# Optimization experiments

Hardware: AMD Instinct MI355X
Metric: run time of the kernel (lower is better)

## Reference

```python
import jax, jax.numpy as jnp
import numpy as np
from jax import lax

VOCAB, E, T, B, LABELS = 50000, 256, 512, 32, 16


def setup_inputs() -> dict:
    key = jax.random.key(0)
    ks = jax.random.split(key, 10)
    inputs = jax.random.randint(ks[0], (B, T), 0, VOCAB)
    emb_table = jax.random.normal(ks[1], (VOCAB, E), jnp.float32) * 0.02
    # Original torch code samples fresh randn weights at every timestep:
    # faithful parameterization is a stacked [T, E, E] weight per matrix.
    Wl = jax.random.normal(ks[2], (T, E, E), jnp.float32)
    Wsl = jax.random.normal(ks[3], (T, E, E), jnp.float32)
    Wr = jax.random.normal(ks[4], (T, E, E), jnp.float32)
    Wsr = jax.random.normal(ks[5], (T, E, E), jnp.float32)
    e_prev0 = jax.random.normal(ks[6], (B, E), jnp.float32)   # embedding_previous init (randn)
    e_foll0 = jax.random.normal(ks[7], (B, E), jnp.float32)   # embedding_following init (randn)
    fc_w = jax.random.normal(ks[8], (LABELS, 3 * E), jnp.float32) * 0.02
    fc_b = jnp.zeros((LABELS,), jnp.float32)
    return {"inputs": inputs, "emb_table": emb_table, "Wl": Wl, "Wsl": Wsl,
            "Wr": Wr, "Wsr": Wsr, "e_prev0": e_prev0, "e_foll0": e_foll0,
            "fc_w": fc_w, "fc_b": fc_b}


def _context_scan(W, Ws, emb_seq, e0):
    # W, Ws: [T, E, E]; emb_seq: [T, B, E] (order in which embeddings feed the recurrence)
    # c_i = tanh(c_{i-1} @ W_i + e_prev @ Ws_i); e_prev starts at e0 then trails emb_seq.
    c0 = jnp.zeros_like(e0)

    def step(carry, xs):
        c_prev, e_prev = carry
        W_i, Ws_i, emb_i = xs
        c = jnp.tanh(c_prev @ W_i + e_prev @ Ws_i)
        return (c, emb_i), c

    _, ctx = lax.scan(step, (c0, e0), (W, Ws, emb_seq))
    return ctx  # [T, B, E]


def reference(inputs, emb_table, Wl, Wsl, Wr, Wsr, e_prev0, e_foll0, fc_w, fc_b):
    emb = emb_table[inputs]                 # [B, T, E]
    emb_t = jnp.transpose(emb, (1, 0, 2))   # [T, B, E]
    left = _context_scan(Wl, Wsl, emb_t, e_prev0)                 # [T, B, E]
    right = _context_scan(Wr, Wsr, emb_t[::-1], e_foll0)[::-1]    # [T, B, E] (reversed order)
    out = jnp.concatenate([left, emb_t, right], axis=-1)          # [T, B, 3E]
    out = jnp.transpose(out, (1, 0, 2))                           # [B, T, 3E]
    pooled = jnp.max(out, axis=1)                                 # [B, 3E]
    # dropout in eval mode: identity
    return pooled @ fc_w.T + fc_b                                 # [B, LABELS]
```

## Files before the change

kernel.cpp:

```cpp
#include <hip/hip_runtime.h>
#include <cstdint>
#include <cstddef>

#define T_ 512
#define B_ 32
#define E_ 256
#define NLAB 16

typedef __attribute__((ext_vector_type(8))) short short8;
typedef __attribute__((ext_vector_type(4))) float f32x4;
typedef __attribute__((ext_vector_type(16))) float f32x16;
typedef __attribute__((ext_vector_type(2))) long long2_t;
typedef __attribute__((ext_vector_type(4))) int int4v;
typedef __attribute__((ext_vector_type(8))) int int8v;

static __device__ __forceinline__ unsigned short f2bf(float f) {
    unsigned u = __float_as_uint(f);
    u = (u + 0x7fffu + ((u >> 16) & 1u)) >> 16;
    return (unsigned short)u;
}

static __device__ __forceinline__ unsigned f2fp8(float x) {
    unsigned u = __float_as_uint(x);
    unsigned sign = (u >> 31) << 7;
    unsigned mag = u & 0x7fffffffu;
    if (mag >= 0x43e00000u) return sign | 0x7eu;
    if (mag < 0x3c800000u) {
        float v = fabsf(x) * 512.0f;
        int r = (int)rintf(v);
        return sign | (unsigned)r;
    }
    unsigned lsb = (mag >> 20) & 1u;
    mag += 0x7ffffu + lsb;
    unsigned exp8 = mag >> 23;
    return sign | (((exp8 - 120u) << 3) | ((mag >> 20) & 7u));
}

static __device__ __forceinline__ unsigned pk_fp8(float a, float b) {
#if __has_builtin(__builtin_amdgcn_cvt_pk_fp8_f32)
    return (unsigned)__builtin_amdgcn_cvt_pk_fp8_f32(a, b, 0, false);
#else
    return f2fp8(a) | (f2fp8(b) << 8);
#endif
}
static __device__ __forceinline__ unsigned pk4_fp8(float a, float b, float c, float d) {
#if __has_builtin(__builtin_amdgcn_cvt_pk_fp8_f32)
    int lo = __builtin_amdgcn_cvt_pk_fp8_f32(a, b, 0, false);
    return (unsigned)__builtin_amdgcn_cvt_pk_fp8_f32(c, d, lo, true);
#else
    return f2fp8(a) | (f2fp8(b) << 8) | (f2fp8(c) << 16) | (f2fp8(d) << 24);
#endif
}

static __device__ __forceinline__ unsigned q4(float x) {
    float a = fabsf(x);
    unsigned c = (a >= 0.25f) + (a >= 0.75f) + (a >= 1.25f) + (a >= 1.75f) +
                 (a >= 2.5f) + (a >= 3.5f) + (a >= 5.0f);
    return c | ((__float_as_uint(x) >> 28) & 8u);
}

static __device__ __forceinline__ float sig_act(float x) {
    float d = __builtin_fmaf(x, x, 1.0f);
#if __has_builtin(__builtin_amdgcn_rsqf)
    float r = __builtin_amdgcn_rsqf(d);
#else
    float r = rsqrtf(d);
#endif
    return x * r;
}

static __device__ __forceinline__ short8 gather_bfrag_f32(const float* Wt, int kt, int nt, int lane) {
    const float* p = Wt + (size_t)(kt * 16 + 8 * (lane >> 5)) * E_ + nt * 32 + (lane & 31);
    short8 r;
#pragma unroll
    for (int j = 0; j < 8; ++j) {
        float v = __builtin_nontemporal_load(p);
        r[j] = (short)f2bf(v);
        p += E_;
    }
    return r;
}
static __device__ __forceinline__ short8 gather_afrag_rows(const float* rowbase, int kt, int lane) {
    const float* p = rowbase + kt * 16 + 8 * (lane >> 5);
    f32x4 v0 = *(const f32x4*)p;
    f32x4 v1 = *(const f32x4*)(p + 4);
    short8 r;
#pragma unroll
    for (int j = 0; j < 4; ++j) r[j] = (short)f2bf(v0[j]);
#pragma unroll
    for (int j = 0; j < 4; ++j) r[4 + j] = (short)f2bf(v1[j]);
    return r;
}
static __device__ __forceinline__ short8 lds_afrag_bf16(const unsigned short* c_buf, int kt, int lane) {
    int b = lane & 31;
    int byte = (b * 512 + (kt * 16 + 8 * (lane >> 5)) * 2) ^ ((b & 7) << 4);
    return *(const short8*)((const char*)c_buf + byte);
}

static __device__ __forceinline__ void produce_w(
        const float* __restrict__ Wl, const float* __restrict__ Wr,
        unsigned char* __restrict__ wfrag, int d, int t, int tid) {
    int lane = tid & 63, w = tid >> 6;
    const float* W = (d ? Wr : Wl) + (size_t)t * E_ * E_;
    int f = w * 32 + (lane & 31);
    int hh = lane >> 5;
    unsigned char* dst = wfrag + (size_t)(d * T_ + t) * 32768 + w * 4096 + lane * 16;
#pragma unroll
    for (int i = 0; i < 4; ++i) {
        const float* p = W + (size_t)(64 * i + 32 * hh) * E_ + f;
        int4v out;
#pragma unroll
        for (int dw = 0; dw < 4; ++dw) {
            unsigned v = 0;
#pragma unroll
            for (int b = 0; b < 4; ++b) {
                float v0 = __builtin_nontemporal_load(p + (size_t)(dw * 8 + 2 * b) * E_);
                float v1 = __builtin_nontemporal_load(p + (size_t)(dw * 8 + 2 * b + 1) * E_);
                v |= (q4(v0) | (q4(v1) << 4)) << (8 * b);
            }
            out[dw] = (int)v;
        }
        *(int4v*)(dst + i * 1024) = out;
    }
}
static __device__ __forceinline__ void produce_z(
        const int* __restrict__ inputs, const float* __restrict__ emb,
        const float* __restrict__ Wsl, const float* __restrict__ Wsr,
        const float* __restrict__ e_prev0, const float* __restrict__ e_foll0,
        unsigned char* __restrict__ zfrag, int d, int t, int tid) {
    int lane = tid & 63, w = tid >> 6;
    const float* Ws = (d ? Wsr : Wsl) + (size_t)t * E_ * E_;
    int b = lane & 31;
    const float* rowbase;
    if (t == 0) {
        rowbase = (d ? e_foll0 : e_prev0) + b * E_;
    } else {
        int tok = inputs[b * T_ + (d ? (T_ - t) : (t - 1))];
        rowbase = emb + (size_t)tok * E_;
    }
    f32x16 acc;
#pragma unroll
    for (int r = 0; r < 16; ++r) acc[r] = 0.0f;
#pragma unroll 2
    for (int kt = 0; kt < 16; ++kt) {
        short8 a = gather_afrag_rows(rowbase, kt, lane);
        short8 bf = gather_bfrag_f32(Ws, kt, w, lane);
        acc = __builtin_amdgcn_mfma_f32_32x32x16_bf16(a, bf, acc, 0, 0, 0);
    }
    unsigned char* zp = zfrag + (size_t)(d * T_ + t) * 8192 + w * 1024;
    int fb = lane & 31;
    int hc = (fb >> 3) & 1;
    int bytepos = (fb >> 4) * 8 + (fb & 7);
    int hz = lane >> 5;
#pragma unroll
    for (int q = 0; q < 8; ++q) {
        unsigned p2 = pk_fp8(acc[2 * q], acc[2 * q + 1]);
        int r0 = 2 * q, r1 = 2 * q + 1;
        int b0 = (r0 & 3) + 8 * (r0 >> 2) + 4 * hz;
        int b1 = (r1 & 3) + 8 * (r1 >> 2) + 4 * hz;
        zp[(32 * hc + b0) * 16 + bytepos] = (unsigned char)p2;
        zp[(32 * hc + b1) * 16 + bytepos] = (unsigned char)(p2 >> 8);
    }
}

__global__ void __launch_bounds__(512, 1) fused_kernel(
        const int* __restrict__ inputs, const float* __restrict__ emb,
        const float* __restrict__ Wl, const float* __restrict__ Wsl,
        const float* __restrict__ Wr, const float* __restrict__ Wsr,
        const float* __restrict__ e_prev0, const float* __restrict__ e_foll0,
        unsigned char* __restrict__ wfrag, unsigned char* __restrict__ zfrag,
        float* __restrict__ pmax_out, int* __restrict__ chunkcnt) {
    int tid = threadIdx.x;

    if (blockIdx.x >= 2) {
        int task = blockIdx.x - 2;
        int d = task >> 9, t = task & 511;
        produce_w(Wl, Wr, wfrag, d, t, tid);
        produce_z(inputs, emb, Wsl, Wsr, e_prev0, e_foll0, zfrag, d, t, tid);
        asm volatile("s_waitcnt vmcnt(0)" ::: "memory");
        __syncthreads();
        if (tid == 0) {
            __hip_atomic_fetch_add(&chunkcnt[(d << 5) | (t >> 4)], 1,
                                   __ATOMIC_RELEASE, __HIP_MEMORY_SCOPE_AGENT);
        }
        return;
    }

    extern __shared__ unsigned char smem[];
    unsigned char* cb0 = smem;
    unsigned char* cb1 = smem + 8448;

    int d = blockIdx.x;
    int lane = tid & 63, w = tid >> 6;
    int hh = lane >> 5;
    int m5 = lane & 31;
    const unsigned char* wg = wfrag + (size_t)d * T_ * 32768 + w * 4096 + lane * 16;
    const unsigned char* zg = zfrag + (size_t)d * T_ * 8192 + w * 1024 + lane * 16;
    const int cb32 = d << 5;

    long aI1 = 0, aI2 = 0;
    {
        int j1 = m5 - 8 * hh;
        if (m5 < 16 && j1 >= 0 && j1 < 8) aI1 = (long)0x38 << (8 * j1);
        int j2 = m5 - 16 - 8 * hh;
        if (m5 >= 16 && j2 >= 0 && j2 < 8) aI2 = (long)0x38 << (8 * j2);
    }

    const unsigned char* crd0 = cb0 + m5 * 264 + 32 * hh;
    const unsigned char* crd1 = cb1 + m5 * 264 + 32 * hh;
    unsigned char* cwr0 = cb0 + m5 * 264 + w * 32 + 4 * hh;
    unsigned char* cwr1 = cb1 + m5 * 264 + w * 32 + 4 * hh;

    f32x16 lmax;
#pragma unroll
    for (int r = 0; r < 16; ++r) lmax[r] = -1e30f;
    f32x16 ZEROV;
#pragma unroll
    for (int r = 0; r < 16; ++r) ZEROV[r] = 0.0f;

    int4v wbA[4], wbB[4];
    long2_t zbA, zbB;

#define VERIFY(cidx)                                                          \
    while (__hip_atomic_load(&chunkcnt[cb32 + (cidx)], __ATOMIC_ACQUIRE,      \
                             __HIP_MEMORY_SCOPE_AGENT) != 16) {}

#define LOADB(tt, WB, ZB)                                                     \
    {                                                                         \
        const unsigned char* wp_ = wg + (size_t)(tt) * 32768;                 \
        WB[0] = *(const int4v*)(wp_);                                         \
        WB[1] = *(const int4v*)(wp_ + 1024);                                  \
        WB[2] = *(const int4v*)(wp_ + 2048);                                  \
        WB[3] = *(const int4v*)(wp_ + 3072);                                  \
        ZB = *(const long2_t*)(zg + (size_t)(tt) * 8192);                     \
    }

#define STEP(tt, WCUR, ZCUR, WNXT, ZNXT, CRD, CWR, DOISSUE)                   \
    {                                                                         \
        if (DOISSUE) LOADB((tt) + 1, WNXT, ZNXT);                             \
        f32x16 acc = __builtin_amdgcn_mfma_f32_32x32x16_fp8_fp8(              \
            aI1, ZCUR[0], ZEROV, 0, 0, 0);                                    \
        acc = __builtin_amdgcn_mfma_f32_32x32x16_fp8_fp8(aI2, ZCUR[1], acc,   \
                                                         0, 0, 0);            \
        if ((tt) > 0) {                                                       \
            _Pragma("unroll")                                                 \
            for (int i_ = 0; i_ < 4; ++i_) {                                  \
                int8v av_ = {WCUR[i_][0], WCUR[i_][1], WCUR[i_][2],           \
                             WCUR[i_][3], 0, 0, 0, 0};                        \
                long c0_ = *(const long*)((CRD) + i_ * 64);                   \
                long c1_ = *(const long*)((CRD) + i_ * 64 + 8);               \
                long c2_ = *(const long*)((CRD) + i_ * 64 + 16);              \
                long c3_ = *(const long*)((CRD) + i_ * 64 + 24);              \
                int8v bv_;                                                    \
                bv_[0] = (int)c0_; bv_[1] = (int)(c0_ >> 32);                 \
                bv_[2] = (int)c1_; bv_[3] = (int)(c1_ >> 32);                 \
                bv_[4] = (int)c2_; bv_[5] = (int)(c2_ >> 32);                 \
                bv_[6] = (int)c3_; bv_[7] = (int)(c3_ >> 32);                 \
                acc = __builtin_amdgcn_mfma_scale_f32_32x32x64_f8f6f4(        \
                    av_, bv_, acc, 4 , 0 , 0, 127, 0, 127); \
            }                                                                 \
        }                                                                     \
        _Pragma("unroll")                                                     \
        for (int r = 0; r < 16; ++r) lmax[r] = fmaxf(lmax[r], acc[r]);        \
        _Pragma("unroll")                                                     \
        for (int q_ = 0; q_ < 4; ++q_) {                                      \
            float t0_ = sig_act(acc[4 * q_ + 0]);                             \
            float t1_ = sig_act(acc[4 * q_ + 1]);                             \
            float t2_ = sig_act(acc[4 * q_ + 2]);                             \
            float t3_ = sig_act(acc[4 * q_ + 3]);                             \
            *(unsigned*)((CWR) + q_ * 8) = pk4_fp8(t0_, t1_, t2_, t3_);       \
        }                                                                     \
        asm volatile("s_waitcnt lgkmcnt(0)" ::: "memory");                    \
        __builtin_amdgcn_s_barrier();                                         \
        asm volatile("" ::: "memory");                                        \
    }

    VERIFY(0);
    VERIFY(1);
    LOADB(0, wbA, zbA);

    for (int tb = 0; tb < 496; tb += 16) {
        if (tb) { VERIFY((tb >> 4) + 1); }
#pragma unroll
        for (int k = 0; k < 16; k += 2) {
            STEP(tb + k, wbA, zbA, wbB, zbB, crd0, cwr1, 1);
            STEP(tb + k + 1, wbB, zbB, wbA, zbA, crd1, cwr0, 1);
        }
    }
#pragma unroll
    for (int k = 0; k < 14; k += 2) {
        STEP(496 + k, wbA, zbA, wbB, zbB, crd0, cwr1, 1);
        STEP(497 + k, wbB, zbB, wbA, zbA, crd1, cwr0, 1);
    }
    STEP(510, wbA, zbA, wbB, zbB, crd0, cwr1, 1);
    STEP(511, wbB, zbB, wbA, zbA, crd1, cwr0, 0);
#undef STEP
#undef LOADB
#undef VERIFY

    float* pm = pmax_out + (((size_t)d * 8 + w) * 64 + lane) * 16;
#pragma unroll
    for (int r = 0; r < 16; ++r) pm[r] = lmax[r];
}

__global__ void zero_flags_kernel(int* __restrict__ chunkcnt) {
    chunkcnt[threadIdx.x] = 0;
}

__global__ void __launch_bounds__(512) chain_lite_kernel(
        const int* __restrict__ inputs, const float* __restrict__ emb,
        const float* __restrict__ Wl, const float* __restrict__ Wsl,
        const float* __restrict__ Wr, const float* __restrict__ Wsr,
        const float* __restrict__ e_prev0, const float* __restrict__ e_foll0,
        float* __restrict__ pmax_out) {
    __shared__ unsigned short c_buf[32 * 256 + 32];
    int d = blockIdx.x;
    int tid = threadIdx.x, lane = tid & 63, w = tid >> 6;
    const float* Wc = (d ? Wr : Wl);
    const float* Wsc = (d ? Wsr : Wsl);
    const float* e0 = (d ? e_foll0 : e_prev0);
    f32x16 lmax;
#pragma unroll
    for (int r = 0; r < 16; ++r) lmax[r] = -1e30f;

    for (int t = 0; t < T_; ++t) {
        f32x16 acc;
#pragma unroll
        for (int r = 0; r < 16; ++r) acc[r] = 0.0f;
        int b = lane & 31;
        const float* rowbase;
        if (t == 0) {
            rowbase = e0 + b * E_;
        } else {
            int tok = inputs[b * T_ + (d ? (T_ - t) : (t - 1))];
            rowbase = emb + (size_t)tok * E_;
        }
        const float* Ws = Wsc + (size_t)t * E_ * E_;
#pragma unroll 2
        for (int kt = 0; kt < 16; ++kt) {
            short8 a = gather_afrag_rows(rowbase, kt, lane);
            short8 bf = gather_bfrag_f32(Ws, kt, w, lane);
            acc = __builtin_amdgcn_mfma_f32_32x32x16_bf16(a, bf, acc, 0, 0, 0);
        }
        if (t > 0) {
            short8 bf[16];
            const float* Wt = Wc + (size_t)t * E_ * E_;
#pragma unroll 2
            for (int kt = 0; kt < 16; ++kt) bf[kt] = gather_bfrag_f32(Wt, kt, w, lane);
            __syncthreads();
#pragma unroll
            for (int kt = 0; kt < 16; ++kt) {
                short8 a = lds_afrag_bf16(c_buf, kt, lane);
                acc = __builtin_amdgcn_mfma_f32_32x32x16_bf16(a, bf[kt], acc, 0, 0, 0);
            }
        }
#pragma unroll
        for (int r = 0; r < 16; ++r) {
            lmax[r] = fmaxf(lmax[r], acc[r]);
            acc[r] = sig_act(acc[r]);
        }
        __syncthreads();
        {
            int n = w * 32 + (lane & 31);
#pragma unroll
            for (int r = 0; r < 16; ++r) {
                int b2 = (r & 3) + 8 * (r >> 2) + 4 * (lane >> 5);
                int byte = (b2 * 512 + n * 2) ^ ((b2 & 7) << 4);
                *(unsigned short*)((char*)c_buf + byte) = f2bf(acc[r]);
            }
        }
        __syncthreads();
    }
    int f = w * 32 + (lane & 31);
    int wv = f >> 5, fb = f & 31;
    int hh_t = (fb >> 2) & 1;
    int r_t = (fb & 3) + 4 * (fb >> 3);
#pragma unroll
    for (int r = 0; r < 16; ++r) {
        int bt = (r & 3) + 8 * (r >> 2) + 4 * (lane >> 5);
        pmax_out[(((size_t)d * 8 + wv) * 64 + (bt + 32 * hh_t)) * 16 + r_t] = lmax[r];
    }
}

__global__ void __launch_bounds__(256) finalize_kernel(
        const int* __restrict__ inputs, const float* __restrict__ emb,
        const float* __restrict__ pmax, const float* __restrict__ fc_w,
        const float* __restrict__ fc_b, float* __restrict__ out) {
    __shared__ float pooled[3 * E_];
    __shared__ float partial[NLAB][17];
    int b = blockIdx.x, e = threadIdx.x;

    float m = -1e30f;
    const int* tr = inputs + b * T_;
#pragma unroll 4
    for (int t = 0; t < T_; ++t) {
        int tok = tr[t];
        m = fmaxf(m, emb[(size_t)tok * E_ + e]);
    }
    pooled[E_ + e] = m;

    int fb = e & 31, wv = e >> 5;
    int hh = (fb >> 2) & 1;
    int r = (fb & 3) + 4 * (fb >> 3);
    int ln = b + 32 * hh;
    pooled[e] = tanhf(pmax[(((size_t)0 * 8 + wv) * 64 + ln) * 16 + r]);
    pooled[2 * E_ + e] = tanhf(pmax[(((size_t)1 * 8 + wv) * 64 + ln) * 16 + r]);
    __syncthreads();

    int l = e & 15, seg = e >> 4;
    float s = 0.0f;
    const float* wrow = fc_w + (size_t)l * (3 * E_) + seg * 48;
    const float* pp = pooled + seg * 48;
#pragma unroll 8
    for (int j = 0; j < 48; ++j) s += pp[j] * wrow[j];
    partial[l][seg] = s;
    __syncthreads();
    if (e < NLAB) {
        float acc = fc_b[e];
#pragma unroll
        for (int k = 0; k < 16; ++k) acc += partial[e][k];
        out[b * NLAB + e] = acc;
    }
}

extern "C" void kernel_launch(void* const* d_in, const int* in_sizes, int n_in,
                              void* d_out, int out_size, void* d_ws, size_t ws_size,
                              hipStream_t stream) {
    (void)in_sizes; (void)n_in; (void)out_size;
    const int* inputs = (const int*)d_in[0];
    const float* emb = (const float*)d_in[1];
    const float* Wl = (const float*)d_in[2];
    const float* Wsl = (const float*)d_in[3];
    const float* Wr = (const float*)d_in[4];
    const float* Wsr = (const float*)d_in[5];
    const float* e0p = (const float*)d_in[6];
    const float* e0f = (const float*)d_in[7];
    const float* fcw = (const float*)d_in[8];
    const float* fcb = (const float*)d_in[9];
    float* out = (float*)d_out;

    const size_t w4_bytes = (size_t)2 * T_ * 32768;
    const size_t z8_bytes = (size_t)2 * T_ * 8192;
    const size_t pm_bytes = (size_t)2 * 8 * 64 * 16 * 4;
    const size_t fl_bytes = 64 * sizeof(int);
    char* ws = (char*)d_ws;

    const int chain_lds = 16896;

    if (ws_size >= w4_bytes + z8_bytes + pm_bytes + fl_bytes) {
        unsigned char* wfrag = (unsigned char*)ws;
        unsigned char* zfrag = (unsigned char*)(ws + w4_bytes);
        float* pmax = (float*)(ws + w4_bytes + z8_bytes);
        int* chunkcnt = (int*)(ws + w4_bytes + z8_bytes + pm_bytes);
        (void)hipFuncSetAttribute((const void*)fused_kernel,
                                  hipFuncAttributeMaxDynamicSharedMemorySize, chain_lds);
        zero_flags_kernel<<<1, 64, 0, stream>>>(chunkcnt);
        fused_kernel<<<1026, 512, chain_lds, stream>>>(
            inputs, emb, Wl, Wsl, Wr, Wsr, e0p, e0f, wfrag, zfrag, pmax, chunkcnt);
        finalize_kernel<<<32, 256, 0, stream>>>(inputs, emb, pmax, fcw, fcb, out);
    } else {
        float* pmax = (float*)ws;
        chain_lite_kernel<<<2, 512, 0, stream>>>(inputs, emb, Wl, Wsl, Wr, Wsr, e0p, e0f,
                                                 pmax);
        finalize_kernel<<<32, 256, 0, stream>>>(inputs, emb, pmax, fcw, fcb, out);
    }
}
```

Measured before the change: 615.8 us.

## Interleave producer tasks, split MFMA chains, skip flag polls, move embedding max into producers

Producer blocks now interleave the two directions (task&1 selects direction), so both recurrence chains get their early timesteps produced at the same time. A global per-direction completion counter lets the chain stop polling per-chunk flags once every chunk is ready. The recurrent MFMAs are split into two independent accumulators to shorten the dependent MFMA chain on the serial critical path. The embedding max-pool moves from the finalize kernel into the last 32 producer blocks, so the tail kernel only does the FC layer. The cost is an extra atomic per producer block and more accumulator registers.

```diff
diff --git a/kernel.cpp b/kernel.cpp
--- a/kernel.cpp
+++ b/kernel.cpp
@@ -169,12 +169,14 @@
         const float* __restrict__ Wr, const float* __restrict__ Wsr,
         const float* __restrict__ e_prev0, const float* __restrict__ e_foll0,
         unsigned char* __restrict__ wfrag, unsigned char* __restrict__ zfrag,
-        float* __restrict__ pmax_out, int* __restrict__ chunkcnt) {
+        float* __restrict__ pmax_out, int* __restrict__ chunkcnt,
+        float* __restrict__ midmax) {
     int tid = threadIdx.x;
+    extern __shared__ unsigned char smem[];
 
     if (blockIdx.x >= 2) {
         int task = blockIdx.x - 2;
-        int d = task >> 9, t = task & 511;
+        int d = task & 1, t = task >> 1;
         produce_w(Wl, Wr, wfrag, d, t, tid);
         produce_z(inputs, emb, Wsl, Wsr, e_prev0, e_foll0, zfrag, d, t, tid);
         asm volatile("s_waitcnt vmcnt(0)" ::: "memory");
@@ -182,11 +184,27 @@
         if (tid == 0) {
             __hip_atomic_fetch_add(&chunkcnt[(d << 5) | (t >> 4)], 1,
                                    __ATOMIC_RELEASE, __HIP_MEMORY_SCOPE_AGENT);
+            __hip_atomic_fetch_add(&chunkcnt[64 + d], 1,
+                                   __ATOMIC_RELEASE, __HIP_MEMORY_SCOPE_AGENT);
+        }
+        if (d == 1 && t >= 480) {
+            int b = t - 480;
+            int e = tid & 255, half = tid >> 8;
+            const int* tr = inputs + b * T_;
+            float m = -1e30f;
+#pragma unroll 4
+            for (int k = 0; k < 256; ++k) {
+                int tok = tr[half * 256 + k];
+                m = fmaxf(m, emb[(size_t)tok * E_ + e]);
+            }
+            float* mm = (float*)smem;
+            mm[half * 256 + e] = m;
+            __syncthreads();
+            if (tid < 256) midmax[b * 256 + tid] = fmaxf(mm[tid], mm[256 + tid]);
         }
         return;
     }
 
-    extern __shared__ unsigned char smem[];
     unsigned char* cb0 = smem;
     unsigned char* cb1 = smem + 8448;
 
@@ -220,10 +238,15 @@
 
     int4v wbA[4], wbB[4];
     long2_t zbA, zbB;
+    int alldone = 0;
 
 #define VERIFY(cidx)                                                          \
-    while (__hip_atomic_load(&chunkcnt[cb32 + (cidx)], __ATOMIC_ACQUIRE,      \
-                             __HIP_MEMORY_SCOPE_AGENT) != 16) {}
+    if (!alldone) {                                                           \
+        while (__hip_atomic_load(&chunkcnt[cb32 + (cidx)], __ATOMIC_ACQUIRE,  \
+                                 __HIP_MEMORY_SCOPE_AGENT) != 16) {}          \
+        alldone = (__hip_atomic_load(&chunkcnt[64 + d], __ATOMIC_ACQUIRE,     \
+                                     __HIP_MEMORY_SCOPE_AGENT) == 512);       \
+    }
 
 #define LOADB(tt, WB, ZB)                                                     \
     {                                                                         \
@@ -238,28 +261,59 @@
 #define STEP(tt, WCUR, ZCUR, WNXT, ZNXT, CRD, CWR, DOISSUE)                   \
     {                                                                         \
         if (DOISSUE) LOADB((tt) + 1, WNXT, ZNXT);                             \
-        f32x16 acc = __builtin_amdgcn_mfma_f32_32x32x16_fp8_fp8(              \
+        f32x16 accP = __builtin_amdgcn_mfma_f32_32x32x16_fp8_fp8(             \
             aI1, ZCUR[0], ZEROV, 0, 0, 0);                                    \
-        acc = __builtin_amdgcn_mfma_f32_32x32x16_fp8_fp8(aI2, ZCUR[1], acc,   \
-                                                         0, 0, 0);            \
+        f32x16 accQ = __builtin_amdgcn_mfma_f32_32x32x16_fp8_fp8(             \
+            aI2, ZCUR[1], ZEROV, 0, 0, 0);                                    \
+        f32x16 acc;                                                           \
         if ((tt) > 0) {                                                       \
-            _Pragma("unroll")                                                 \
-            for (int i_ = 0; i_ < 4; ++i_) {                                  \
-                int8v av_ = {WCUR[i_][0], WCUR[i_][1], WCUR[i_][2],           \
-                             WCUR[i_][3], 0, 0, 0, 0};                        \
-                long c0_ = *(const long*)((CRD) + i_ * 64);                   \
-                long c1_ = *(const long*)((CRD) + i_ * 64 + 8);               \
-                long c2_ = *(const long*)((CRD) + i_ * 64 + 16);              \
-                long c3_ = *(const long*)((CRD) + i_ * 64 + 24);              \
-                int8v bv_;                                                    \
-                bv_[0] = (int)c0_; bv_[1] = (int)(c0_ >> 32);                 \
-                bv_[2] = (int)c1_; bv_[3] = (int)(c1_ >> 32);                 \
-                bv_[4] = (int)c2_; bv_[5] = (int)(c2_ >> 32);                 \
-                bv_[6] = (int)c3_; bv_[7] = (int)(c3_ >> 32);                 \
-                acc = __builtin_amdgcn_mfma_scale_f32_32x32x64_f8f6f4(        \
-                    av_, bv_, acc, 4 , 0 , 0, 127, 0, 127); \
-            }                                                                 \
+            long c0_ = *(const long*)(CRD);                                   \
+            long c1_ = *(const long*)((CRD) + 8);                             \
+            long c2_ = *(const long*)((CRD) + 16);                            \
+            long c3_ = *(const long*)((CRD) + 24);                            \
+            long c4_ = *(const long*)((CRD) + 64);                            \
+            long c5_ = *(const long*)((CRD) + 72);                            \
+            long c6_ = *(const long*)((CRD) + 80);                            \
+            long c7_ = *(const long*)((CRD) + 88);                            \
+            long c8_ = *(const long*)((CRD) + 128);                           \
+            long c9_ = *(const long*)((CRD) + 136);                           \
+            long ca_ = *(const long*)((CRD) + 144);                           \
+            long cb_ = *(const long*)((CRD) + 152);                           \
+            long cc_ = *(const long*)((CRD) + 192);                           \
+            long cd_ = *(const long*)((CRD) + 200);                           \
+            long ce_ = *(const long*)((CRD) + 208);                           \
+            long cf_ = *(const long*)((CRD) + 216);                           \
+            int8v a0_ = {WCUR[0][0], WCUR[0][1], WCUR[0][2], WCUR[0][3],      \
+                         0, 0, 0, 0};                                         \
+            int8v a1_ = {WCUR[1][0], WCUR[1][1], WCUR[1][2], WCUR[1][3],      \
+                         0, 0, 0, 0};                                         \
+            int8v a2_ = {WCUR[2][0], WCUR[2][1], WCUR[2][2], WCUR[2][3],      \
+                         0, 0, 0, 0};                                         \
+            int8v a3_ = {WCUR[3][0], WCUR[3][1], WCUR[3][2], WCUR[3][3],      \
+                         0, 0, 0, 0};                                         \
+            int8v b0_ = {(int)c0_, (int)(c0_ >> 32), (int)c1_,                \
+                         (int)(c1_ >> 32), (int)c2_, (int)(c2_ >> 32),        \
+                         (int)c3_, (int)(c3_ >> 32)};                         \
+            int8v b1_ = {(int)c4_, (int)(c4_ >> 32), (int)c5_,                \
+                         (int)(c5_ >> 32), (int)c6_, (int)(c6_ >> 32),        \
+                         (int)c7_, (int)(c7_ >> 32)};                         \
+            int8v b2_ = {(int)c8_, (int)(c8_ >> 32), (int)c9_,                \
+                         (int)(c9_ >> 32), (int)ca_, (int)(ca_ >> 32),        \
+                         (int)cb_, (int)(cb_ >> 32)};                         \
+            int8v b3_ = {(int)cc_, (int)(cc_ >> 32), (int)cd_,                \
+                         (int)(cd_ >> 32), (int)ce_, (int)(ce_ >> 32),        \
+                         (int)cf_, (int)(cf_ >> 32)};                         \
+            accP = __builtin_amdgcn_mfma_scale_f32_32x32x64_f8f6f4(           \
+                a0_, b0_, accP, 4, 0, 0, 127, 0, 127);                        \
+            accQ = __builtin_amdgcn_mfma_scale_f32_32x32x64_f8f6f4(           \
+                a1_, b1_, accQ, 4, 0, 0, 127, 0, 127);                        \
+            accP = __builtin_amdgcn_mfma_scale_f32_32x32x64_f8f6f4(           \
+                a2_, b2_, accP, 4, 0, 0, 127, 0, 127);                        \
+            accQ = __builtin_amdgcn_mfma_scale_f32_32x32x64_f8f6f4(           \
+                a3_, b3_, accQ, 4, 0, 0, 127, 0, 127);                        \
         }                                                                     \
+        _Pragma("unroll")                                                     \
+        for (int r = 0; r < 16; ++r) acc[r] = accP[r] + accQ[r];              \
         _Pragma("unroll")                                                     \
         for (int r = 0; r < 16; ++r) lmax[r] = fmaxf(lmax[r], acc[r]);        \
         _Pragma("unroll")                                                     \
@@ -304,7 +358,8 @@
 }
 
 __global__ void zero_flags_kernel(int* __restrict__ chunkcnt) {
-    chunkcnt[threadIdx.x] = 0;
+    int i = threadIdx.x;
+    if (i < 66) chunkcnt[i] = 0;
 }
 
 __global__ void __launch_bounds__(512) chain_lite_kernel(
@@ -383,6 +438,40 @@
 }
 
 __global__ void __launch_bounds__(256) finalize_kernel(
+        const float* __restrict__ midmax, const float* __restrict__ pmax,
+        const float* __restrict__ fc_w, const float* __restrict__ fc_b,
+        float* __restrict__ out) {
+    __shared__ float pooled[3 * E_];
+    __shared__ float partial[NLAB][17];
+    int b = blockIdx.x, e = threadIdx.x;
+
+    pooled[E_ + e] = midmax[b * 256 + e];
+
+    int fb = e & 31, wv = e >> 5;
+    int hh = (fb >> 2) & 1;
+    int r = (fb & 3) + 4 * (fb >> 3);
+    int ln = b + 32 * hh;
+    pooled[e] = tanhf(pmax[(((size_t)0 * 8 + wv) * 64 + ln) * 16 + r]);
+    pooled[2 * E_ + e] = tanhf(pmax[(((size_t)1 * 8 + wv) * 64 + ln) * 16 + r]);
+    __syncthreads();
+
+    int l = e & 15, seg = e >> 4;
+    float s = 0.0f;
+    const float* wrow = fc_w + (size_t)l * (3 * E_) + seg * 48;
+    const float* pp = pooled + seg * 48;
+#pragma unroll 8
+    for (int j = 0; j < 48; ++j) s += pp[j] * wrow[j];
+    partial[l][seg] = s;
+    __syncthreads();
+    if (e < NLAB) {
+        float acc = fc_b[e];
+#pragma unroll
+        for (int k = 0; k < 16; ++k) acc += partial[e][k];
+        out[b * NLAB + e] = acc;
+    }
+}
+
+__global__ void __launch_bounds__(256) finalize_lite_kernel(
         const int* __restrict__ inputs, const float* __restrict__ emb,
         const float* __restrict__ pmax, const float* __restrict__ fc_w,
         const float* __restrict__ fc_b, float* __restrict__ out) {
@@ -442,26 +531,29 @@
     const size_t w4_bytes = (size_t)2 * T_ * 32768;
     const size_t z8_bytes = (size_t)2 * T_ * 8192;
     const size_t pm_bytes = (size_t)2 * 8 * 64 * 16 * 4;
-    const size_t fl_bytes = 64 * sizeof(int);
+    const size_t fl_bytes = 512;
+    const size_t mm_bytes = (size_t)B_ * E_ * 4;
     char* ws = (char*)d_ws;
 
     const int chain_lds = 16896;
 
-    if (ws_size >= w4_bytes + z8_bytes + pm_bytes + fl_bytes) {
+    if (ws_size >= w4_bytes + z8_bytes + pm_bytes + fl_bytes + mm_bytes) {
         unsigned char* wfrag = (unsigned char*)ws;
         unsigned char* zfrag = (unsigned char*)(ws + w4_bytes);
         float* pmax = (float*)(ws + w4_bytes + z8_bytes);
         int* chunkcnt = (int*)(ws + w4_bytes + z8_bytes + pm_bytes);
+        float* midmax = (float*)(ws + w4_bytes + z8_bytes + pm_bytes + fl_bytes);
         (void)hipFuncSetAttribute((const void*)fused_kernel,
                                   hipFuncAttributeMaxDynamicSharedMemorySize, chain_lds);
-        zero_flags_kernel<<<1, 64, 0, stream>>>(chunkcnt);
+        zero_flags_kernel<<<1, 128, 0, stream>>>(chunkcnt);
         fused_kernel<<<1026, 512, chain_lds, stream>>>(
-            inputs, emb, Wl, Wsl, Wr, Wsr, e0p, e0f, wfrag, zfrag, pmax, chunkcnt);
-        finalize_kernel<<<32, 256, 0, stream>>>(inputs, emb, pmax, fcw, fcb, out);
+            inputs, emb, Wl, Wsl, Wr, Wsr, e0p, e0f, wfrag, zfrag, pmax, chunkcnt,
+            midmax);
+        finalize_kernel<<<32, 256, 0, stream>>>(midmax, pmax, fcw, fcb, out);
     } else {
         float* pmax = (float*)ws;
         chain_lite_kernel<<<2, 512, 0, stream>>>(inputs, emb, Wl, Wsl, Wr, Wsr, e0p, e0f,
                                                  pmax);
-        finalize_kernel<<<32, 256, 0, stream>>>(inputs, emb, pmax, fcw, fcb, out);
-    }
-}
+        finalize_lite_kernel<<<32, 256, 0, stream>>>(inputs, emb, pmax, fcw, fcb, out);
+    }
+}
```

Measured after the change: 521.7 us. 15.3% less time.
